# Kernel optimization log

Hardware: AMD Instinct MI355X
Metric: run time of the kernel (lower is better)

The kernel has to match this reference:

```python
import jax, jax.numpy as jnp
import numpy as np

D_MODEL = 1024
N_HEAD = 16
D_K = D_MODEL // N_HEAD


def setup_inputs() -> dict:
    key = jax.random.key(0)
    ks = jax.random.split(key, 11)
    B, S = 2, 2048
    std = 1.0 / np.sqrt(D_MODEL)
    inp = {
        "Q": jax.random.normal(ks[0], (B, S, D_MODEL), jnp.float32),
        "K": jax.random.normal(ks[1], (B, S, D_MODEL), jnp.float32),
        "V": jax.random.normal(ks[2], (B, S, D_MODEL), jnp.float32),
        "Wq": jax.random.normal(ks[3], (D_MODEL, D_MODEL), jnp.float32) * std,
        "bq": jnp.zeros((D_MODEL,), jnp.float32),
        "Wk": jax.random.normal(ks[4], (D_MODEL, D_MODEL), jnp.float32) * std,
        "bk": jnp.zeros((D_MODEL,), jnp.float32),
        "Wv": jax.random.normal(ks[5], (D_MODEL, D_MODEL), jnp.float32) * std,
        "bv": jnp.zeros((D_MODEL,), jnp.float32),
        "Wo": jax.random.normal(ks[6], (D_MODEL, D_MODEL), jnp.float32) * std,
        "bo": jnp.zeros((D_MODEL,), jnp.float32),
    }
    return inp


def _split_heads(x):
    # [B, S, D] -> [B, H, S, d_k]
    B, S, _ = x.shape
    return x.reshape(B, S, N_HEAD, D_K).transpose(0, 2, 1, 3)


def reference(Q, K, V, Wq, bq, Wk, bk, Wv, bv, Wo, bo):
    q = _split_heads(Q @ Wq.T + bq)   # [B,H,S,dk]
    k = _split_heads(K @ Wk.T + bk)
    v = _split_heads(V @ Wv.T + bv)
    scale = 1.0 / jnp.sqrt(jnp.float32(D_K))
    scores = jnp.einsum("bhqd,bhkd->bhqk", q, k) * scale
    attn = jax.nn.softmax(scores, axis=-1)
    ctx = jnp.einsum("bhqk,bhkd->bhqd", attn, v)  # [B,H,S,dk]
    B, H, S, dk = ctx.shape
    ctx = ctx.transpose(0, 2, 1, 3).reshape(B, S, H * dk)
    return ctx @ Wo.T + bo
```

## Files before the change

kernel.cpp:

```cpp
#include <hip/hip_runtime.h>
#include <hip/hip_bf16.h>
#include <cstdint>
#include <cstddef>
#include <cmath>

typedef __attribute__((ext_vector_type(8))) short short8;
typedef __attribute__((ext_vector_type(4))) short short4_t;
typedef __attribute__((ext_vector_type(4))) float f32x4;

constexpr int B_ = 2, S_ = 2048, H_ = 16, DK_ = 64, DM_ = 1024;

__device__ inline unsigned short f2bf(float x) {
  union { float f; unsigned u; } c; c.f = x;
  unsigned r = c.u + 0x7FFF + ((c.u >> 16) & 1);
  return (unsigned short)(r >> 16);
}

__device__ inline float ex2(float x) {
#if __has_builtin(__builtin_amdgcn_exp2f)
  return __builtin_amdgcn_exp2f(x);
#else
  return exp2f(x);
#endif
}

__device__ inline unsigned pkbf(float lo, float hi) {
  unsigned u;
  asm("v_cvt_pk_bf16_f32 %0, %1, %2" : "=v"(u) : "v"(lo), "v"(hi));
  return u;
}

__device__ inline f32x4 mfma16(short8 a, short8 b, f32x4 c) {
  return __builtin_amdgcn_mfma_f32_16x16x32_bf16(a, b, c, 0, 0, 0);
}

__device__ inline void glds16(const unsigned short* g, unsigned short* l) {
  __builtin_amdgcn_global_load_lds(
      (const __attribute__((address_space(1))) unsigned int*)g,
      (__attribute__((address_space(3))) unsigned int*)l, 16, 0, 0);
}

__global__ __launch_bounds__(256) void cvt_all(
    const float* __restrict__ Q, const float* __restrict__ K,
    const float* __restrict__ V, const float* __restrict__ Wq,
    const float* __restrict__ Wk, const float* __restrict__ Wv,
    const float* __restrict__ Wo, unsigned short* __restrict__ Qb,
    unsigned short* __restrict__ Kb, unsigned short* __restrict__ Vb,
    unsigned short* __restrict__ Wqb, unsigned short* __restrict__ Wkb,
    unsigned short* __restrict__ Wvb, unsigned short* __restrict__ Wob) {
  int bid = blockIdx.x;
  const float* in; unsigned short* out; int off;
  if (bid < 4096)       { in = Q;  out = Qb;  off = bid; }
  else if (bid < 8192)  { in = K;  out = Kb;  off = bid - 4096; }
  else if (bid < 12288) { in = V;  out = Vb;  off = bid - 8192; }
  else if (bid < 13312) { in = Wq; out = Wqb; off = bid - 12288; }
  else if (bid < 14336) { in = Wk; out = Wkb; off = bid - 13312; }
  else if (bid < 15360) { in = Wv; out = Wvb; off = bid - 14336; }
  else                  { in = Wo; out = Wob; off = bid - 15360; }
  int i = off * 256 + threadIdx.x;
  float4 f = ((const float4*)in)[i];
  uint2 o;
  o.x = pkbf(f.x, f.y);
  o.y = pkbf(f.z, f.w);
  ((uint2*)out)[i] = o;
}

__device__ inline void store_out(float* p, float v) { *p = v; }
__device__ inline void store_out(unsigned short* p, float v) { *p = f2bf(v); }

template <typename OUT_T>
__device__ inline void gemm_body(const unsigned short* __restrict__ A,
                                 const unsigned short* __restrict__ Bw,
                                 const float* __restrict__ bias,
                                 OUT_T* __restrict__ C, float cscale,
                                 int bm, int bn) {
  constexpr int Kd = 1024, Nd = 1024;
  __shared__ unsigned short As[128][64];
  __shared__ unsigned short Bs[64][64];

  const int tid = threadIdx.x;
  const int lane = tid & 63, wave = tid >> 6;
  const int li = lane & 15, lg = lane >> 4;
  const int wm = wave >> 1, wn = wave & 1;

  const f32x4 zero4 = {0.f, 0.f, 0.f, 0.f};
  f32x4 acc[4][2];
#pragma unroll
  for (int i = 0; i < 4; i++)
#pragma unroll
    for (int j = 0; j < 2; j++) acc[i][j] = zero4;

  const int stg_row = tid >> 3;
  const int stg_col = (tid & 7) * 8;
  const unsigned short* Ag = A + (size_t)(bm * 128 + stg_row) * Kd + stg_col;
  const unsigned short* Bg = Bw + (size_t)(bn * 64 + stg_row) * Kd + stg_col;

  for (int kt = 0; kt < Kd; kt += 64) {
#pragma unroll
    for (int i = 0; i < 4; i++)
      glds16(Ag + (size_t)(i * 32) * Kd + kt, &As[i * 32 + stg_row][stg_col]);
#pragma unroll
    for (int i = 0; i < 2; i++)
      glds16(Bg + (size_t)(i * 32) * Kd + kt, &Bs[i * 32 + stg_row][stg_col]);
    __syncthreads();

    short8 af[4][2], bf[2][2];
#pragma unroll
    for (int kb = 0; kb < 2; kb++) {
#pragma unroll
      for (int i = 0; i < 4; i++)
        af[i][kb] = *(const short8*)&As[wm * 64 + i * 16 + li][kb * 32 + lg * 8];
#pragma unroll
      for (int j = 0; j < 2; j++)
        bf[j][kb] = *(const short8*)&Bs[wn * 32 + j * 16 + li][kb * 32 + lg * 8];
    }
#pragma unroll
    for (int kb = 0; kb < 2; kb++)
#pragma unroll
      for (int i = 0; i < 4; i++)
#pragma unroll
        for (int j = 0; j < 2; j++)
          acc[i][j] = mfma16(af[i][kb], bf[j][kb], acc[i][j]);
    __syncthreads();
  }

#pragma unroll
  for (int j = 0; j < 2; j++) {
    int col = bn * 64 + wn * 32 + j * 16 + li;
    float bv = bias[col];
#pragma unroll
    for (int i = 0; i < 4; i++) {
      int row0 = bm * 128 + wm * 64 + i * 16 + lg * 4;
#pragma unroll
      for (int r = 0; r < 4; r++)
        store_out(&C[(size_t)(row0 + r) * Nd + col], (acc[i][j][r] + bv) * cscale);
    }
  }
}

__global__ __launch_bounds__(256) void gemm_qkv(
    const unsigned short* __restrict__ Aq, const unsigned short* __restrict__ Ak,
    const unsigned short* __restrict__ Av, const unsigned short* __restrict__ Bq,
    const unsigned short* __restrict__ Bk, const unsigned short* __restrict__ Bv,
    const float* __restrict__ bq, const float* __restrict__ bk,
    const float* __restrict__ bv, unsigned short* __restrict__ Cq,
    unsigned short* __restrict__ Ck, unsigned short* __restrict__ Cv,
    float qscale) {
  const int n = blockIdx.x;
  const int xcd = n & 7, m = n >> 3;
  const int z = m >> 6, idx = m & 63;
  const int bm = xcd * 4 + (idx >> 4), bn = idx & 15;
  const unsigned short* A = z == 0 ? Aq : z == 1 ? Ak : Av;
  const unsigned short* Bw = z == 0 ? Bq : z == 1 ? Bk : Bv;
  const float* bi = z == 0 ? bq : z == 1 ? bk : bv;
  unsigned short* C = z == 0 ? Cq : z == 1 ? Ck : Cv;
  gemm_body(A, Bw, bi, C, z == 0 ? qscale : 1.0f, bm, bn);
}

__global__ __launch_bounds__(256) void gemm_out(
    const unsigned short* __restrict__ A, const unsigned short* __restrict__ Bw,
    const float* __restrict__ bias, float* __restrict__ C) {
  const int n = blockIdx.x;
  const int xcd = n & 7, m = n >> 3;
  const int bm = xcd * 4 + (m >> 4), bn = m & 15;
  gemm_body(A, Bw, bias, C, 1.0f, bm, bn);
}

__global__ __launch_bounds__(256) void attn_fwd(
    const unsigned short* __restrict__ q, const unsigned short* __restrict__ k,
    const unsigned short* __restrict__ v, unsigned short* __restrict__ ctx) {
  __shared__ unsigned short Ks[2][64][64];
  __shared__ unsigned short Vt[64][72];
  __shared__ unsigned short Ps[4][16][72];

  const int tid = threadIdx.x;
  const int lane = tid & 63, wave = tid >> 6;
  const int li = lane & 15, lg = lane >> 4;
  const int n = blockIdx.x;
  const int xcd = n & 7, m = n >> 3;
  const int bh = xcd * 4 + (m & 3);
  const int qt = m >> 2;
  const int b = bh >> 4, h = bh & 15;

  const unsigned short* qg =
      q + (size_t)(b * S_ + qt * 64 + wave * 16 + li) * DM_ + h * DK_;
  short8 qf[2];
  qf[0] = *(const short8*)(qg + lg * 8);
  qf[1] = *(const short8*)(qg + 32 + lg * 8);

  const f32x4 zero4 = {0.f, 0.f, 0.f, 0.f};
  f32x4 po[4];
#pragma unroll
  for (int d = 0; d < 4; d++) po[d] = zero4;
  float m_i = -1e30f, l_i = 0.f;

  const int srow = tid >> 3;
  const int sc = tid & 7;
  const int scs = (sc ^ (srow & 7)) * 8;
  const unsigned short* kg = k + (size_t)(b * S_) * DM_ + h * DK_;

  const int vkey2 = (tid & 31) * 2;
  const int vd0 = (tid >> 5) * 8;
  const unsigned short* vg = v + (size_t)(b * S_) * DM_ + h * DK_;

  const int NT = S_ / 64;

  glds16(kg + (size_t)srow * DM_ + scs, &Ks[0][srow][sc * 8]);
  glds16(kg + (size_t)(32 + srow) * DM_ + scs, &Ks[0][32 + srow][sc * 8]);
  short8 t0, t1;
  {
    const unsigned short* vp = vg + (size_t)vkey2 * DM_ + vd0;
    t0 = *(const short8*)(vp);
    t1 = *(const short8*)(vp + DM_);
  }

  for (int kt = 0; kt < NT; kt++) {
    const int buf = kt & 1;
    asm volatile("s_waitcnt vmcnt(0)" ::: "memory");
    __builtin_amdgcn_sched_barrier(0);
    __builtin_amdgcn_s_barrier();
    __builtin_amdgcn_sched_barrier(0);

#pragma unroll
    for (int j = 0; j < 8; j++) {
      unsigned w = (unsigned)(unsigned short)t0[j] |
                   ((unsigned)(unsigned short)t1[j] << 16);
      *(unsigned*)&Vt[vd0 + j][vkey2] = w;
    }

    if (kt + 1 < NT) {
      const unsigned short* kgt = kg + (size_t)((kt + 1) * 64) * DM_;
      glds16(kgt + (size_t)srow * DM_ + scs, &Ks[buf ^ 1][srow][sc * 8]);
      glds16(kgt + (size_t)(32 + srow) * DM_ + scs, &Ks[buf ^ 1][32 + srow][sc * 8]);
      const unsigned short* vp = vg + (size_t)((kt + 1) * 64 + vkey2) * DM_ + vd0;
      t0 = *(const short8*)(vp);
      t1 = *(const short8*)(vp + DM_);
    }

    asm volatile("s_waitcnt lgkmcnt(0)" ::: "memory");
    __builtin_amdgcn_sched_barrier(0);
    __builtin_amdgcn_s_barrier();
    __builtin_amdgcn_sched_barrier(0);

    f32x4 sacc[4];
#pragma unroll
    for (int cb = 0; cb < 4; cb++) sacc[cb] = zero4;
#pragma unroll
    for (int cb = 0; cb < 4; cb++)
#pragma unroll
      for (int kb = 0; kb < 2; kb++) {
        short8 kf = *(const short8*)
            &Ks[buf][cb * 16 + li][((kb * 4 + lg) ^ (li & 7)) * 8];
        sacc[cb] = mfma16(kf, qf[kb], sacc[cb]);
      }

    float mx;
    {
      f32x4 t01, t23;
#pragma unroll
      for (int r = 0; r < 4; r++) {
        t01[r] = fmaxf(sacc[0][r], sacc[1][r]);
        t23[r] = fmaxf(sacc[2][r], sacc[3][r]);
      }
      float a = fmaxf(fmaxf(t01[0], t01[1]), fmaxf(t01[2], t01[3]));
      float c = fmaxf(fmaxf(t23[0], t23[1]), fmaxf(t23[2], t23[3]));
      mx = fmaxf(a, c);
    }
    mx = fmaxf(mx, __shfl_xor(mx, 16));
    mx = fmaxf(mx, __shfl_xor(mx, 32));

    if (!__all(mx - m_i <= 8.0f)) {
      float mn = fmaxf(m_i, mx);
      float al = ex2(m_i - mn);
      m_i = mn;
      l_i *= al;
#pragma unroll
      for (int d = 0; d < 4; d++)
#pragma unroll
        for (int r = 0; r < 4; r++) po[d][r] *= al;
    }

    float p[4][4];
#pragma unroll
    for (int cb = 0; cb < 4; cb++)
#pragma unroll
      for (int r = 0; r < 4; r++) p[cb][r] = ex2(sacc[cb][r] - m_i);
    float s0 = (p[0][0] + p[0][1]) + (p[0][2] + p[0][3]);
    float s1 = (p[1][0] + p[1][1]) + (p[1][2] + p[1][3]);
    float s2 = (p[2][0] + p[2][1]) + (p[2][2] + p[2][3]);
    float s3 = (p[3][0] + p[3][1]) + (p[3][2] + p[3][3]);
    float sum = (s0 + s1) + (s2 + s3);
    sum += __shfl_xor(sum, 16);
    sum += __shfl_xor(sum, 32);
    l_i += sum;

#pragma unroll
    for (int cb = 0; cb < 4; cb++) {
      uint2 w;
      w.x = pkbf(p[cb][0], p[cb][1]);
      w.y = pkbf(p[cb][2], p[cb][3]);
      *(uint2*)&Ps[wave][li][cb * 16 + lg * 4] = w;
    }

    short8 pf0 = *(const short8*)&Ps[wave][li][lg * 8];
    short8 pf1 = *(const short8*)&Ps[wave][li][32 + lg * 8];
#pragma unroll
    for (int d = 0; d < 4; d++) {
      short8 vf0 = *(const short8*)&Vt[d * 16 + li][lg * 8];
      short8 vf1 = *(const short8*)&Vt[d * 16 + li][32 + lg * 8];
      po[d] = mfma16(vf0, pf0, po[d]);
      po[d] = mfma16(vf1, pf1, po[d]);
    }
  }

  float rl = 1.0f / l_i;
  unsigned short* cg =
      ctx + (size_t)(b * S_ + qt * 64 + wave * 16 + li) * DM_ + h * DK_;
#pragma unroll
  for (int db = 0; db < 4; db++) {
    uint2 w;
    w.x = pkbf(po[db][0] * rl, po[db][1] * rl);
    w.y = pkbf(po[db][2] * rl, po[db][3] * rl);
    *(uint2*)(cg + db * 16 + lg * 4) = w;
  }
}

extern "C" void kernel_launch(void* const* d_in, const int* in_sizes, int n_in,
                              void* d_out, int out_size, void* d_ws, size_t ws_size,
                              hipStream_t stream) {
  const float* Q  = (const float*)d_in[0];
  const float* Kx = (const float*)d_in[1];
  const float* V  = (const float*)d_in[2];
  const float* Wq = (const float*)d_in[3];
  const float* bq = (const float*)d_in[4];
  const float* Wk = (const float*)d_in[5];
  const float* bk = (const float*)d_in[6];
  const float* Wv = (const float*)d_in[7];
  const float* bv = (const float*)d_in[8];
  const float* Wo = (const float*)d_in[9];
  const float* bo = (const float*)d_in[10];
  float* out = (float*)d_out;

  char* ws = (char*)d_ws;
  const size_t MB = 1ull << 20;
  unsigned short* Qb  = (unsigned short*)(ws + 0 * MB);
  unsigned short* Kb  = (unsigned short*)(ws + 8 * MB);
  unsigned short* Vb  = (unsigned short*)(ws + 16 * MB);
  unsigned short* Wqb = (unsigned short*)(ws + 24 * MB);
  unsigned short* Wkb = (unsigned short*)(ws + 26 * MB);
  unsigned short* Wvb = (unsigned short*)(ws + 28 * MB);
  unsigned short* Wob = (unsigned short*)(ws + 30 * MB);
  unsigned short* qp  = (unsigned short*)(ws + 32 * MB);
  unsigned short* kp  = (unsigned short*)(ws + 40 * MB);
  unsigned short* vp  = (unsigned short*)(ws + 48 * MB);
  unsigned short* cx  = (unsigned short*)(ws + 56 * MB);

  cvt_all<<<16384, 256, 0, stream>>>(Q, Kx, V, Wq, Wk, Wv, Wo,
                                     Qb, Kb, Vb, Wqb, Wkb, Wvb, Wob);

  gemm_qkv<<<1536, 256, 0, stream>>>(
      Qb, Kb, Vb, Wqb, Wkb, Wvb, bq, bk, bv, qp, kp, vp, 0.18033688f);

  attn_fwd<<<1024, 256, 0, stream>>>(qp, kp, vp, cx);

  gemm_out<<<512, 256, 0, stream>>>(cx, Wob, bo, out);
}
```

Before: 152.0 us.

## Switch attention to 32x32x16 MFMA with 128-query tiles and register-resident P

Rewrites the attention kernel to use 32x32x16 bf16 MFMA instructions, with each wave owning 32 query rows so a block covers 128 queries and the grid is halved. The softmax probabilities are kept in registers and rearranged with cross-half lane shuffles instead of a round trip through the Ps shared-memory buffer. The V transpose in shared memory now uses an XOR swizzle instead of padding. The aim is fewer LDS operations, better K/V reuse per tile load and denser matrix instructions, at the cost of more registers per thread and fewer blocks to fill the CUs.

```diff
diff --git a/kernel.cpp b/kernel.cpp
--- a/kernel.cpp
+++ b/kernel.cpp
@@ -7,6 +7,7 @@
 typedef __attribute__((ext_vector_type(8))) short short8;
 typedef __attribute__((ext_vector_type(4))) short short4_t;
 typedef __attribute__((ext_vector_type(4))) float f32x4;
+typedef __attribute__((ext_vector_type(16))) float f32x16;
 
 constexpr int B_ = 2, S_ = 2048, H_ = 16, DK_ = 64, DM_ = 1024;
 
@@ -32,6 +33,9 @@
 
 __device__ inline f32x4 mfma16(short8 a, short8 b, f32x4 c) {
   return __builtin_amdgcn_mfma_f32_16x16x32_bf16(a, b, c, 0, 0, 0);
+}
+__device__ inline f32x16 mfma32(short8 a, short8 b, f32x16 c) {
+  return __builtin_amdgcn_mfma_f32_32x32x16_bf16(a, b, c, 0, 0, 0);
 }
 
 __device__ inline void glds16(const unsigned short* g, unsigned short* l) {
@@ -170,38 +174,39 @@
     const unsigned short* __restrict__ q, const unsigned short* __restrict__ k,
     const unsigned short* __restrict__ v, unsigned short* __restrict__ ctx) {
   __shared__ unsigned short Ks[2][64][64];
-  __shared__ unsigned short Vt[64][72];
-  __shared__ unsigned short Ps[4][16][72];
+  __shared__ unsigned short Vt[64][64];
 
   const int tid = threadIdx.x;
   const int lane = tid & 63, wave = tid >> 6;
-  const int li = lane & 15, lg = lane >> 4;
+  const int l31 = lane & 31, h = lane >> 5;
   const int n = blockIdx.x;
   const int xcd = n & 7, m = n >> 3;
   const int bh = xcd * 4 + (m & 3);
   const int qt = m >> 2;
-  const int b = bh >> 4, h = bh & 15;
-
-  const unsigned short* qg =
-      q + (size_t)(b * S_ + qt * 64 + wave * 16 + li) * DM_ + h * DK_;
-  short8 qf[2];
-  qf[0] = *(const short8*)(qg + lg * 8);
-  qf[1] = *(const short8*)(qg + 32 + lg * 8);
-
-  const f32x4 zero4 = {0.f, 0.f, 0.f, 0.f};
-  f32x4 po[4];
-#pragma unroll
-  for (int d = 0; d < 4; d++) po[d] = zero4;
+  const int b = bh >> 4, hd = bh & 15;
+
+  const int qrow = qt * 128 + wave * 32 + l31;
+  const unsigned short* qg = q + (size_t)(b * S_ + qrow) * DM_ + hd * DK_;
+  short8 qf[4];
+#pragma unroll
+  for (int t = 0; t < 4; t++) qf[t] = *(const short8*)(qg + t * 16 + h * 8);
+
+  f32x16 po[2];
+#pragma unroll
+  for (int db = 0; db < 2; db++)
+#pragma unroll
+    for (int r = 0; r < 16; r++) po[db][r] = 0.f;
   float m_i = -1e30f, l_i = 0.f;
 
   const int srow = tid >> 3;
   const int sc = tid & 7;
   const int scs = (sc ^ (srow & 7)) * 8;
-  const unsigned short* kg = k + (size_t)(b * S_) * DM_ + h * DK_;
-
-  const int vkey2 = (tid & 31) * 2;
+  const unsigned short* kg = k + (size_t)(b * S_) * DM_ + hd * DK_;
+
+  const int vm = tid & 31;
+  const int vkey2 = vm * 2;
   const int vd0 = (tid >> 5) * 8;
-  const unsigned short* vg = v + (size_t)(b * S_) * DM_ + h * DK_;
+  const unsigned short* vg = v + (size_t)(b * S_) * DM_ + hd * DK_;
 
   const int NT = S_ / 64;
 
@@ -225,7 +230,8 @@
     for (int j = 0; j < 8; j++) {
       unsigned w = (unsigned)(unsigned short)t0[j] |
                    ((unsigned)(unsigned short)t1[j] << 16);
-      *(unsigned*)&Vt[vd0 + j][vkey2] = w;
+      int slot = (vm >> 2) ^ j;
+      *(unsigned*)&Vt[vd0 + j][slot * 8 + (vkey2 & 7)] = w;
     }
 
     if (kt + 1 < NT) {
@@ -242,31 +248,31 @@
     __builtin_amdgcn_s_barrier();
     __builtin_amdgcn_sched_barrier(0);
 
-    f32x4 sacc[4];
-#pragma unroll
-    for (int cb = 0; cb < 4; cb++) sacc[cb] = zero4;
-#pragma unroll
-    for (int cb = 0; cb < 4; cb++)
+    f32x16 sacc[2];
+#pragma unroll
+    for (int kb = 0; kb < 2; kb++)
+#pragma unroll
+      for (int r = 0; r < 16; r++) sacc[kb][r] = 0.f;
+#pragma unroll
+    for (int t = 0; t < 4; t++) {
+      const int slot = ((t << 1) | h) ^ (l31 & 7);
 #pragma unroll
       for (int kb = 0; kb < 2; kb++) {
-        short8 kf = *(const short8*)
-            &Ks[buf][cb * 16 + li][((kb * 4 + lg) ^ (li & 7)) * 8];
-        sacc[cb] = mfma16(kf, qf[kb], sacc[cb]);
-      }
+        short8 kf = *(const short8*)&Ks[buf][kb * 32 + l31][slot * 8];
+        sacc[kb] = mfma32(kf, qf[t], sacc[kb]);
+      }
+    }
 
     float mx;
     {
-      f32x4 t01, t23;
-#pragma unroll
-      for (int r = 0; r < 4; r++) {
-        t01[r] = fmaxf(sacc[0][r], sacc[1][r]);
-        t23[r] = fmaxf(sacc[2][r], sacc[3][r]);
-      }
-      float a = fmaxf(fmaxf(t01[0], t01[1]), fmaxf(t01[2], t01[3]));
-      float c = fmaxf(fmaxf(t23[0], t23[1]), fmaxf(t23[2], t23[3]));
+      float a = -1e30f, c = -1e30f;
+#pragma unroll
+      for (int r = 0; r < 16; r += 2) {
+        a = fmaxf(a, fmaxf(sacc[0][r], sacc[0][r + 1]));
+        c = fmaxf(c, fmaxf(sacc[1][r], sacc[1][r + 1]));
+      }
       mx = fmaxf(a, c);
     }
-    mx = fmaxf(mx, __shfl_xor(mx, 16));
     mx = fmaxf(mx, __shfl_xor(mx, 32));
 
     if (!__all(mx - m_i <= 8.0f)) {
@@ -275,54 +281,69 @@
       m_i = mn;
       l_i *= al;
 #pragma unroll
-      for (int d = 0; d < 4; d++)
-#pragma unroll
-        for (int r = 0; r < 4; r++) po[d][r] *= al;
-    }
-
-    float p[4][4];
-#pragma unroll
-    for (int cb = 0; cb < 4; cb++)
-#pragma unroll
-      for (int r = 0; r < 4; r++) p[cb][r] = ex2(sacc[cb][r] - m_i);
-    float s0 = (p[0][0] + p[0][1]) + (p[0][2] + p[0][3]);
-    float s1 = (p[1][0] + p[1][1]) + (p[1][2] + p[1][3]);
-    float s2 = (p[2][0] + p[2][1]) + (p[2][2] + p[2][3]);
-    float s3 = (p[3][0] + p[3][1]) + (p[3][2] + p[3][3]);
+      for (int db = 0; db < 2; db++)
+#pragma unroll
+        for (int r = 0; r < 16; r++) po[db][r] *= al;
+    }
+
+    float s0 = 0.f, s1 = 0.f, s2 = 0.f, s3 = 0.f;
+#pragma unroll
+    for (int kb = 0; kb < 2; kb++)
+#pragma unroll
+      for (int r = 0; r < 16; r += 4) {
+        float p0 = ex2(sacc[kb][r] - m_i);
+        float p1 = ex2(sacc[kb][r + 1] - m_i);
+        float p2 = ex2(sacc[kb][r + 2] - m_i);
+        float p3 = ex2(sacc[kb][r + 3] - m_i);
+        sacc[kb][r] = p0; sacc[kb][r + 1] = p1;
+        sacc[kb][r + 2] = p2; sacc[kb][r + 3] = p3;
+        s0 += p0; s1 += p1; s2 += p2; s3 += p3;
+      }
     float sum = (s0 + s1) + (s2 + s3);
-    sum += __shfl_xor(sum, 16);
     sum += __shfl_xor(sum, 32);
     l_i += sum;
 
-#pragma unroll
-    for (int cb = 0; cb < 4; cb++) {
-      uint2 w;
-      w.x = pkbf(p[cb][0], p[cb][1]);
-      w.y = pkbf(p[cb][2], p[cb][3]);
-      *(uint2*)&Ps[wave][li][cb * 16 + lg * 4] = w;
-    }
-
-    short8 pf0 = *(const short8*)&Ps[wave][li][lg * 8];
-    short8 pf1 = *(const short8*)&Ps[wave][li][32 + lg * 8];
-#pragma unroll
-    for (int d = 0; d < 4; d++) {
-      short8 vf0 = *(const short8*)&Vt[d * 16 + li][lg * 8];
-      short8 vf1 = *(const short8*)&Vt[d * 16 + li][32 + lg * 8];
-      po[d] = mfma16(vf0, pf0, po[d]);
-      po[d] = mfma16(vf1, pf1, po[d]);
+    unsigned u[2][4][2];
+#pragma unroll
+    for (int kb = 0; kb < 2; kb++)
+#pragma unroll
+      for (int qd = 0; qd < 4; qd++) {
+        u[kb][qd][0] = pkbf(sacc[kb][4 * qd], sacc[kb][4 * qd + 1]);
+        u[kb][qd][1] = pkbf(sacc[kb][4 * qd + 2], sacc[kb][4 * qd + 3]);
+      }
+
+#pragma unroll
+    for (int t = 0; t < 4; t++) {
+      const int kb = t >> 1, qe = (t & 1) * 2;
+      unsigned X0 = u[kb][qe][0], X1 = u[kb][qe][1];
+      unsigned Y0 = u[kb][qe + 1][0], Y1 = u[kb][qe + 1][1];
+      unsigned sX0 = __shfl_xor(X0, 32), sX1 = __shfl_xor(X1, 32);
+      unsigned sY0 = __shfl_xor(Y0, 32), sY1 = __shfl_xor(Y1, 32);
+      union { unsigned w[4]; short8 v8; } fr;
+      fr.w[0] = h ? sY0 : X0;
+      fr.w[1] = h ? sY1 : X1;
+      fr.w[2] = h ? Y0 : sX0;
+      fr.w[3] = h ? Y1 : sX1;
+      const int slot = ((t << 1) | h) ^ (l31 & 7);
+#pragma unroll
+      for (int db = 0; db < 2; db++) {
+        short8 vf = *(const short8*)&Vt[db * 32 + l31][slot * 8];
+        po[db] = mfma32(vf, fr.v8, po[db]);
+      }
     }
   }
 
   float rl = 1.0f / l_i;
-  unsigned short* cg =
-      ctx + (size_t)(b * S_ + qt * 64 + wave * 16 + li) * DM_ + h * DK_;
-#pragma unroll
-  for (int db = 0; db < 4; db++) {
-    uint2 w;
-    w.x = pkbf(po[db][0] * rl, po[db][1] * rl);
-    w.y = pkbf(po[db][2] * rl, po[db][3] * rl);
-    *(uint2*)(cg + db * 16 + lg * 4) = w;
-  }
+  unsigned short* cg = ctx + (size_t)(b * S_ + qrow) * DM_ + hd * DK_;
+#pragma unroll
+  for (int db = 0; db < 2; db++)
+#pragma unroll
+    for (int rq = 0; rq < 4; rq++) {
+      uint2 w2;
+      w2.x = pkbf(po[db][4 * rq] * rl, po[db][4 * rq + 1] * rl);
+      w2.y = pkbf(po[db][4 * rq + 2] * rl, po[db][4 * rq + 3] * rl);
+      *(uint2*)(cg + db * 32 + 8 * rq + 4 * h) = w2;
+    }
 }
 
 extern "C" void kernel_launch(void* const* d_in, const int* in_sizes, int n_in,
@@ -361,7 +382,7 @@
   gemm_qkv<<<1536, 256, 0, stream>>>(
       Qb, Kb, Vb, Wqb, Wkb, Wvb, bq, bk, bv, qp, kp, vp, 0.18033688f);
 
-  attn_fwd<<<1024, 256, 0, stream>>>(qp, kp, vp, cx);
+  attn_fwd<<<512, 256, 0, stream>>>(qp, kp, vp, cx);
 
   gemm_out<<<512, 256, 0, stream>>>(cx, Wob, bo, out);
 }
```

New measurement: 148.2 us. -2.5%, faster.
